# Kernel optimization log

Measured on AMD Instinct MI355X. Metric: run time of the kernel, lower is better.

The kernel has to match this reference:

```python
import jax, jax.numpy as jnp
import numpy as np

N_HEADS = 16
BLOCK_SIZE = 256


def _rope(x):
    # x: [B, H, L, d] ; matches torch RotaryPositionalEmbedding (interleave-split then concat)
    B, H, L, d = x.shape
    inv_freq = 1.0 / (10000.0 ** (jnp.arange(0, d, 2, dtype=jnp.float32) / d))
    t = jnp.arange(L, dtype=jnp.float32)[:, None] * inv_freq[None, :]  # [L, d/2]
    cos, sin = jnp.cos(t), jnp.sin(t)
    x1, x2 = x[..., 0::2], x[..., 1::2]
    return jnp.concatenate([x1 * cos - x2 * sin, x2 * cos + x1 * sin], axis=-1)


def setup_inputs() -> dict:
    key = jax.random.key(0)
    k1, k2, k3 = jax.random.split(key, 3)
    B, L, D = 2, 4096, 1024
    x = jax.random.normal(k1, (B, L, D), dtype=jnp.float32)
    Wqkv = jax.random.normal(k2, (3 * D, D), dtype=jnp.float32) * 0.02
    Wout = jax.random.normal(k3, (D, D), dtype=jnp.float32) * 0.02
    return {"x": x, "Wqkv": Wqkv, "Wout": Wout}


def reference(x, Wqkv, Wout):
    H, BS = N_HEADS, BLOCK_SIZE
    B, L, D = x.shape
    HD = D // H
    scale = HD ** (-0.5)
    nb = L // BS

    qkv = (x @ Wqkv.T).reshape(B, L, 3, H, HD).transpose(2, 0, 3, 1, 4)  # [3,B,H,L,HD]
    q, k, v = qkv[0], qkv[1], qkv[2]
    q, k = _rope(q), _rope(k)

    # block-diagonal causal attention: only within-block scores are ever unmasked,
    # and fp32 exp(finfo.min - max) == 0, so blockwise softmax == masked full softmax
    qb = q.reshape(B, H, nb, BS, HD)
    kb = k.reshape(B, H, nb, BS, HD)
    vb = v.reshape(B, H, nb, BS, HD)

    att = jnp.einsum('bhnqd,bhnkd->bhnqk', qb, kb) * scale
    causal = jnp.tril(jnp.ones((BS, BS), dtype=bool))
    att = jnp.where(causal, att, jnp.finfo(att.dtype).min)
    att = jax.nn.softmax(att, axis=-1)  # dropout p=0.0 -> identity

    out = jnp.einsum('bhnqk,bhnkd->bhnqd', att, vb)
    out = out.reshape(B, H, L, HD).transpose(0, 2, 1, 3).reshape(B, L, D)
    return out @ Wout.T
```

## Files before the change

kernel.cpp:

```cpp
#include <hip/hip_runtime.h>
#include <hip/hip_bf16.h>
#include <cstdint>
#include <cstddef>

typedef __hip_bfloat16 bf16;
typedef __attribute__((ext_vector_type(8))) short bf16x8;
typedef __attribute__((ext_vector_type(4))) float floatx4;

static constexpr int Bb = 2;
static constexpr int Ls = 4096;
static constexpr int Dm = 1024;
static constexpr int Hn = 16;
static constexpr int HD = 64;
static constexpr int BS = 256;
static constexpr int QKVROW = 3 * Dm;
static constexpr int KRP = 72;

static constexpr size_t NX  = (size_t)8192 * 1024;
static constexpr size_t NQ  = (size_t)8192 * 3072;
static constexpr size_t NW1 = (size_t)3072 * 1024;
static constexpr size_t NW2 = (size_t)1024 * 1024;

__device__ __forceinline__ void async_load16(const void* g, void* l) {
  __builtin_amdgcn_global_load_lds(
      (__attribute__((address_space(1))) void*)(void*)(g),
      (__attribute__((address_space(3))) void*)(l), 16, 0, 0);
}

__device__ __forceinline__ short f2bf(float f) {
  union { __hip_bfloat16 b; short s; } u;
  u.b = __float2bfloat16(f);
  return u.s;
}

__device__ __forceinline__ float bf2f(short s) {
  union { unsigned u; float f; } v;
  v.u = ((unsigned)(unsigned short)s) << 16;
  return v.f;
}

__device__ __forceinline__ bf16x8 load8(const float* p) {
  const float4 f0 = *(const float4*)(const void*)p;
  const float4 f1 = *(const float4*)(const void*)(p + 4);
  bf16x8 r;
  r[0] = f2bf(f0.x); r[1] = f2bf(f0.y); r[2] = f2bf(f0.z); r[3] = f2bf(f0.w);
  r[4] = f2bf(f1.x); r[5] = f2bf(f1.y); r[6] = f2bf(f1.z); r[7] = f2bf(f1.w);
  return r;
}

__device__ __forceinline__ void storeC(bf16* C, size_t idx, float v) {
  C[idx] = __float2bfloat16(v);
}
__device__ __forceinline__ void storeC(float* C, size_t idx, float v) {
  C[idx] = v;
}

__global__ void cvt3_kernel(const float* __restrict__ x, const float* __restrict__ w1,
                            const float* __restrict__ w2, bf16* __restrict__ xb,
                            bf16* __restrict__ w1b, bf16* __restrict__ w2b) {
  const size_t i = ((size_t)blockIdx.x * 256 + threadIdx.x) * 8;
  if (i < NX) {
    *(bf16x8*)(void*)((short*)(void*)xb + i) = load8(x + i);
  } else if (i < NX + NW1) {
    const size_t k = i - NX;
    *(bf16x8*)(void*)((short*)(void*)w1b + k) = load8(w1 + k);
  } else {
    const size_t k = i - NX - NW1;
    *(bf16x8*)(void*)((short*)(void*)w2b + k) = load8(w2 + k);
  }
}

template <typename TC>
__global__ __launch_bounds__(256) void gemm_bt_async(
    const bf16* __restrict__ A, const bf16* __restrict__ Bm, TC* __restrict__ C,
    int M, int N, int K) {
  __shared__ __align__(16) short sA[128 * 32];
  __shared__ __align__(16) short sB[128 * 32];
  const int tid  = threadIdx.x;
  const int wave = tid >> 6, lane = tid & 63;
  const int quad = lane >> 4, l15 = lane & 15;
  const int tm = blockIdx.y * 128, tn = blockIdx.x * 128;
  const int wm = (wave >> 1) * 64, wn = (wave & 1) * 64;

  floatx4 acc[4][4];
#pragma unroll
  for (int i = 0; i < 4; i++)
#pragma unroll
    for (int j = 0; j < 4; j++) acc[i][j] = {0.f, 0.f, 0.f, 0.f};

  const int srow = tid >> 2;
  const int scol = (tid & 3) * 8;
  const bf16* Ag0 = A + (size_t)(tm + srow) * K + scol;
  const bf16* Ag1 = A + (size_t)(tm + srow + 64) * K + scol;
  const bf16* Bg0 = Bm + (size_t)(tn + srow) * K + scol;
  const bf16* Bg1 = Bm + (size_t)(tn + srow + 64) * K + scol;
  short* sAd0 = sA + tid * 8;
  short* sAd1 = sA + 2048 + tid * 8;
  short* sBd0 = sB + tid * 8;
  short* sBd1 = sB + 2048 + tid * 8;

  for (int kb = 0; kb < K; kb += 32) {
    __syncthreads();
    async_load16(Ag0 + kb, sAd0);
    async_load16(Ag1 + kb, sAd1);
    async_load16(Bg0 + kb, sBd0);
    async_load16(Bg1 + kb, sBd1);
    __syncthreads();

    bf16x8 af[4], bfr[4];
#pragma unroll
    for (int i = 0; i < 4; i++)
      af[i] = *(const bf16x8*)(sA + (wm + i * 16 + l15) * 32 + quad * 8);
#pragma unroll
    for (int j = 0; j < 4; j++)
      bfr[j] = *(const bf16x8*)(sB + (wn + j * 16 + l15) * 32 + quad * 8);
#pragma unroll
    for (int i = 0; i < 4; i++)
#pragma unroll
      for (int j = 0; j < 4; j++)
        acc[i][j] = __builtin_amdgcn_mfma_f32_16x16x32_bf16(af[i], bfr[j], acc[i][j], 0, 0, 0);
  }

#pragma unroll
  for (int i = 0; i < 4; i++)
#pragma unroll
    for (int j = 0; j < 4; j++)
#pragma unroll
      for (int r = 0; r < 4; r++) {
        const int row = tm + wm + i * 16 + quad * 4 + r;
        const int col = tn + wn + j * 16 + l15;
        storeC(C, (size_t)row * N + col, acc[i][j][r]);
      }
}

__device__ __forceinline__ void rope_frag(const bf16* __restrict__ row, int quad,
                                          float l_pos, const float* __restrict__ freq8,
                                          bf16x8* f0, bf16x8* f1) {
  const bf16x8 w0 = *(const bf16x8*)(const void*)(row + quad * 16);
  const bf16x8 w1 = *(const bf16x8*)(const void*)(row + quad * 16 + 8);
#pragma unroll
  for (int j = 0; j < 8; j++) {
    const short s1 = (j < 4) ? w0[2 * j] : w1[2 * (j - 4)];
    const short s2 = (j < 4) ? w0[2 * j + 1] : w1[2 * (j - 4) + 1];
    const float x1 = bf2f(s1), x2 = bf2f(s2);
    const float rev = l_pos * freq8[j];
    const float fr = rev - floorf(rev);
    const float c = __builtin_amdgcn_cosf(fr);
    const float s = __builtin_amdgcn_sinf(fr);
    (*f0)[j] = f2bf(x1 * c - x2 * s);
    (*f1)[j] = f2bf(x2 * c + x1 * s);
  }
}

__global__ __launch_bounds__(256) void attn_kernel(const bf16* __restrict__ qkv,
                                                   bf16* __restrict__ aout) {
  constexpr float SCALE = 0.125f;
  constexpr float LOG2E = 1.4426950408889634f;
  constexpr float INV2PI = 0.15915494309189535f;
  __shared__ __align__(16) short vT[HD * BS];
  __shared__ __align__(16) short kR[BS * KRP];
  __shared__ __align__(16) short pS[4][16 * 64];
  const int blk = blockIdx.x, h = blockIdx.y, b = blockIdx.z;
  const int tid = threadIdx.x;
  const int wave = tid >> 6, lane = tid & 63;
  const int quad = lane >> 4, l15 = lane & 15;
  const size_t row0 = (size_t)(b * Ls + blk * BS);
  const bf16* qkvR = qkv + row0 * QKVROW;

  float freq8[8];
#pragma unroll
  for (int j = 0; j < 8; j++)
    freq8[j] = exp2f(-13.287712379549449f * (float)(2 * (quad * 8 + j)) * (1.0f / 64.0f))
               * INV2PI;

  {
    const bf16* vrow = qkvR + (size_t)tid * QKVROW + 2 * Dm + h * HD;
#pragma unroll
    for (int i = 0; i < 8; i++) {
      bf16x8 vv = *(const bf16x8*)(vrow + i * 8);
#pragma unroll
      for (int e = 0; e < 8; e++) vT[(i * 8 + e) * BS + tid] = vv[e];
    }
  }

  {
    const bf16* krow = qkvR + (size_t)tid * QKVROW + Dm + h * HD;
    bf16x8 kw[8];
#pragma unroll
    for (int t = 0; t < 8; t++) kw[t] = *(const bf16x8*)(krow + t * 8);
    const float pos = (float)(blk * BS + tid);
    short tmp[64];
#pragma unroll
    for (int i = 0; i < 32; i++) {
      const float x1 = bf2f(kw[(2 * i) >> 3][(2 * i) & 7]);
      const float x2 = bf2f(kw[(2 * i + 1) >> 3][(2 * i + 1) & 7]);
      const float fq = exp2f(-13.287712379549449f * (float)(2 * i) * (1.0f / 64.0f)) * INV2PI;
      const float rev = pos * fq;
      const float fr = rev - floorf(rev);
      const float c = __builtin_amdgcn_cosf(fr);
      const float s = __builtin_amdgcn_sinf(fr);
      tmp[i]      = f2bf(x1 * c - x2 * s);
      tmp[i + 32] = f2bf(x2 * c + x1 * s);
    }
#pragma unroll
    for (int t = 0; t < 8; t++)
      *(bf16x8*)(kR + tid * KRP + t * 8) = *(const bf16x8*)(tmp + t * 8);
  }
  __syncthreads();

  short* myP = &pS[wave][0];

  for (int sp = 0; sp < 2; sp++) {
    const int s = sp ? (7 - wave) : wave;
    const int qrow0 = s * 32;
    const int kcmax = s >> 1;

    bf16x8 qf[2][2];
#pragma unroll
    for (int mt = 0; mt < 2; mt++) {
      const int qr = qrow0 + mt * 16 + l15;
      rope_frag(qkvR + (size_t)qr * QKVROW + h * HD, quad,
                (float)(blk * BS + qr), freq8, &qf[mt][0], &qf[mt][1]);
    }

    float m_i[2][4], l_i[2][4];
    floatx4 o[2][4];
#pragma unroll
    for (int mt = 0; mt < 2; mt++)
#pragma unroll
      for (int r = 0; r < 4; r++) { m_i[mt][r] = -1e30f; l_i[mt][r] = 0.f; }
#pragma unroll
    for (int mt = 0; mt < 2; mt++)
#pragma unroll
      for (int nt = 0; nt < 4; nt++) o[mt][nt] = {0.f, 0.f, 0.f, 0.f};

    for (int kc = 0; kc <= kcmax; kc++) {
      floatx4 sc[2][4];
#pragma unroll
      for (int mt = 0; mt < 2; mt++)
#pragma unroll
        for (int nt = 0; nt < 4; nt++) sc[mt][nt] = {0.f, 0.f, 0.f, 0.f};

      bf16x8 kf[4][2];
#pragma unroll
      for (int nt = 0; nt < 4; nt++) {
        const short* kr = kR + (kc * 64 + nt * 16 + l15) * KRP;
        kf[nt][0] = *(const bf16x8*)(kr + quad * 8);
        kf[nt][1] = *(const bf16x8*)(kr + 32 + quad * 8);
      }

#pragma unroll
      for (int mt = 0; mt < 2; mt++)
#pragma unroll
        for (int nt = 0; nt < 4; nt++) {
          sc[mt][nt] = __builtin_amdgcn_mfma_f32_16x16x32_bf16(qf[mt][0], kf[nt][0], sc[mt][nt], 0, 0, 0);
          sc[mt][nt] = __builtin_amdgcn_mfma_f32_16x16x32_bf16(qf[mt][1], kf[nt][1], sc[mt][nt], 0, 0, 0);
        }

      const bool diag = (kc == kcmax);
#pragma unroll
      for (int mt = 0; mt < 2; mt++)
#pragma unroll
        for (int r = 0; r < 4; r++) {
          const int rowg = qrow0 + mt * 16 + quad * 4 + r;
          float cmax = -1e30f;
#pragma unroll
          for (int nt = 0; nt < 4; nt++) {
            float sv = sc[mt][nt][r] * SCALE;
            if (diag && (kc * 64 + nt * 16 + l15 > rowg)) sv = -1e30f;
            sc[mt][nt][r] = sv;
            cmax = fmaxf(cmax, sv);
          }
#pragma unroll
          for (int off = 1; off < 16; off <<= 1)
            cmax = fmaxf(cmax, __shfl_xor(cmax, off, 64));
          const float mold = m_i[mt][r];
          const float mnew = fmaxf(mold, cmax);
          const float alpha = exp2f((mold - mnew) * LOG2E);
          float rsum = 0.f;
#pragma unroll
          for (int nt = 0; nt < 4; nt++) {
            const float p = exp2f((sc[mt][nt][r] - mnew) * LOG2E);
            sc[mt][nt][r] = p;
            rsum += p;
          }
#pragma unroll
          for (int off = 1; off < 16; off <<= 1)
            rsum += __shfl_xor(rsum, off, 64);
          l_i[mt][r] = l_i[mt][r] * alpha + rsum;
          m_i[mt][r] = mnew;
#pragma unroll
          for (int nt = 0; nt < 4; nt++) o[mt][nt][r] *= alpha;
        }

      bf16x8 vf0[4], vf1[4];
#pragma unroll
      for (int nt = 0; nt < 4; nt++) {
        vf0[nt] = *(const bf16x8*)(vT + (nt * 16 + l15) * BS + kc * 64 + quad * 8);
        vf1[nt] = *(const bf16x8*)(vT + (nt * 16 + l15) * BS + kc * 64 + 32 + quad * 8);
      }

#pragma unroll
      for (int mt = 0; mt < 2; mt++) {
#pragma unroll
        for (int nt = 0; nt < 4; nt++)
#pragma unroll
          for (int r = 0; r < 4; r++)
            myP[(quad * 4 + r) * 64 + nt * 16 + l15] = f2bf(sc[mt][nt][r]);
        __asm__ __volatile__("s_waitcnt lgkmcnt(0)" ::: "memory");
        const bf16x8 pf0 = *(const bf16x8*)(myP + l15 * 64 + quad * 8);
        const bf16x8 pf1 = *(const bf16x8*)(myP + l15 * 64 + 32 + quad * 8);
#pragma unroll
        for (int nt = 0; nt < 4; nt++) {
          o[mt][nt] = __builtin_amdgcn_mfma_f32_16x16x32_bf16(pf0, vf0[nt], o[mt][nt], 0, 0, 0);
          o[mt][nt] = __builtin_amdgcn_mfma_f32_16x16x32_bf16(pf1, vf1[nt], o[mt][nt], 0, 0, 0);
        }
        __asm__ __volatile__("s_waitcnt lgkmcnt(0)" ::: "memory");
      }
    }

#pragma unroll
    for (int mt = 0; mt < 2; mt++)
#pragma unroll
      for (int r = 0; r < 4; r++) {
        const float inv = 1.0f / l_i[mt][r];
#pragma unroll
        for (int nt = 0; nt < 4; nt++) {
          const size_t m = row0 + qrow0 + mt * 16 + quad * 4 + r;
          aout[m * Dm + h * HD + nt * 16 + l15] = __float2bfloat16(o[mt][nt][r] * inv);
        }
      }
  }
}

extern "C" void kernel_launch(void* const* d_in, const int* in_sizes, int n_in,
                              void* d_out, int out_size, void* d_ws, size_t ws_size,
                              hipStream_t stream) {
  const float* x    = (const float*)d_in[0];
  const float* Wqkv = (const float*)d_in[1];
  const float* Wout = (const float*)d_in[2];
  float* out = (float*)d_out;

  bf16* xb    = (bf16*)d_ws;
  bf16* qkv   = xb + NX;
  bf16* Wqkvb = qkv + NQ;
  bf16* Woutb = Wqkvb + NW1;
  bf16* attnb = xb;

  cvt3_kernel<<<(NX + NW1 + NW2) / 2048, 256, 0, stream>>>(x, Wqkv, Wout, xb, Wqkvb, Woutb);

  gemm_bt_async<bf16>
      <<<dim3(3072 / 128, 8192 / 128), 256, 0, stream>>>(xb, Wqkvb, qkv, 8192, 3072, 1024);
  attn_kernel<<<dim3(Ls / BS, Hn, Bb), 256, 0, stream>>>(qkv, attnb);
  gemm_bt_async<float>
      <<<dim3(1024 / 128, 8192 / 128), 256, 0, stream>>>(attnb, Woutb, out, 8192, 1024, 1024);
}
```

Before: 234.0 us.

## Rewrite GEMM with 256x128 tiles, triple-buffered async LDS loads and XOR swizzle

The bf16 GEMM used for the QKV and output projections is replaced. The new version uses 512-thread blocks with 256x128 output tiles and a K-step of 64. It keeps three LDS buffers and prefetches two stages ahead, using vmcnt waits and a single barrier per iteration in place of two full syncs. It also XOR-swizzles the LDS layout to avoid bank conflicts and raises wave priority around the MFMA block. The aim is to hide global-load latency and cut barrier and bank-conflict stalls, at the cost of more LDS per block (about 144KB), which may limit occupancy.

```diff
diff --git a/kernel.cpp b/kernel.cpp
--- a/kernel.cpp
+++ b/kernel.cpp
@@ -71,16 +71,38 @@
 }
 
 template <typename TC>
-__global__ __launch_bounds__(256) void gemm_bt_async(
+__global__ __launch_bounds__(512, 2) void gemm_bt_256(
     const bf16* __restrict__ A, const bf16* __restrict__ Bm, TC* __restrict__ C,
     int M, int N, int K) {
-  __shared__ __align__(16) short sA[128 * 32];
-  __shared__ __align__(16) short sB[128 * 32];
-  const int tid  = threadIdx.x;
+  constexpr int BM = 256, BN = 128, BK = 64, NBUF = 3;
+  __shared__ __align__(16) short sA[NBUF][BM * BK];
+  __shared__ __align__(16) short sB[NBUF][BN * BK];
+  const int tid = threadIdx.x;
   const int wave = tid >> 6, lane = tid & 63;
   const int quad = lane >> 4, l15 = lane & 15;
-  const int tm = blockIdx.y * 128, tn = blockIdx.x * 128;
-  const int wm = (wave >> 1) * 64, wn = (wave & 1) * 64;
+  const int wr = wave >> 1, wc = wave & 1;
+  const int tm = blockIdx.y * BM, tn = blockIdx.x * BN;
+  const int xr = (l15 & 7) << 3;
+
+  const int srow = tid >> 3;
+  const int scol = ((tid & 7) ^ (srow & 7)) * 8;
+  const bf16* Ag = A + (size_t)(tm + srow) * K + scol;
+  const bf16* Bg = Bm + (size_t)(tn + srow) * K + scol;
+  short* sAst = &sA[0][0] + tid * 8;
+  short* sBst = &sB[0][0] + tid * 8;
+
+#define STAGE(T, BUF)                                              \
+  do {                                                             \
+    const size_t kb_ = (size_t)(T) * BK;                           \
+    short* sa_ = sAst + (BUF) * (BM * BK);                         \
+    short* sb_ = sBst + (BUF) * (BN * BK);                         \
+    async_load16(Ag + kb_,                   sa_);                 \
+    async_load16(Ag + kb_ + (size_t)64 * K,  sa_ + 4096);          \
+    async_load16(Ag + kb_ + (size_t)128 * K, sa_ + 8192);          \
+    async_load16(Ag + kb_ + (size_t)192 * K, sa_ + 12288);         \
+    async_load16(Bg + kb_,                   sb_);                 \
+    async_load16(Bg + kb_ + (size_t)64 * K,  sb_ + 4096);          \
+  } while (0)
 
   floatx4 acc[4][4];
 #pragma unroll
@@ -88,48 +110,61 @@
 #pragma unroll
     for (int j = 0; j < 4; j++) acc[i][j] = {0.f, 0.f, 0.f, 0.f};
 
-  const int srow = tid >> 2;
-  const int scol = (tid & 3) * 8;
-  const bf16* Ag0 = A + (size_t)(tm + srow) * K + scol;
-  const bf16* Ag1 = A + (size_t)(tm + srow + 64) * K + scol;
-  const bf16* Bg0 = Bm + (size_t)(tn + srow) * K + scol;
-  const bf16* Bg1 = Bm + (size_t)(tn + srow + 64) * K + scol;
-  short* sAd0 = sA + tid * 8;
-  short* sAd1 = sA + 2048 + tid * 8;
-  short* sBd0 = sB + tid * 8;
-  short* sBd1 = sB + 2048 + tid * 8;
-
-  for (int kb = 0; kb < K; kb += 32) {
-    __syncthreads();
-    async_load16(Ag0 + kb, sAd0);
-    async_load16(Ag1 + kb, sAd1);
-    async_load16(Bg0 + kb, sBd0);
-    async_load16(Bg1 + kb, sBd1);
-    __syncthreads();
-
-    bf16x8 af[4], bfr[4];
-#pragma unroll
-    for (int i = 0; i < 4; i++)
-      af[i] = *(const bf16x8*)(sA + (wm + i * 16 + l15) * 32 + quad * 8);
-#pragma unroll
-    for (int j = 0; j < 4; j++)
-      bfr[j] = *(const bf16x8*)(sB + (wn + j * 16 + l15) * 32 + quad * 8);
-#pragma unroll
-    for (int i = 0; i < 4; i++)
-#pragma unroll
-      for (int j = 0; j < 4; j++)
-        acc[i][j] = __builtin_amdgcn_mfma_f32_16x16x32_bf16(af[i], bfr[j], acc[i][j], 0, 0, 0);
-  }
-
-#pragma unroll
-  for (int i = 0; i < 4; i++)
-#pragma unroll
-    for (int j = 0; j < 4; j++)
+  const int nk = K / BK;
+  STAGE(0, 0);
+  STAGE(1, 1);
+  int cur = 0;
+  for (int t = 0; t < nk; ++t) {
+    if (t + 1 < nk)
+      asm volatile("s_waitcnt vmcnt(6)" ::: "memory");
+    else
+      asm volatile("s_waitcnt vmcnt(0)" ::: "memory");
+    __builtin_amdgcn_s_barrier();
+    if (t + 2 < nk) {
+      int pb = cur + 2; if (pb >= NBUF) pb -= NBUF;
+      STAGE(t + 2, pb);
+    }
+
+    const short* aB = &sA[cur][0];
+    const short* bB = &sB[cur][0];
+    bf16x8 af[4][2], bfr[4][2];
+#pragma unroll
+    for (int m = 0; m < 4; m++) {
+      const int row = wr * 64 + m * 16 + l15;
+#pragma unroll
+      for (int ks = 0; ks < 2; ks++)
+        af[m][ks] = *(const bf16x8*)(aB + ((row * 64 + ks * 32 + quad * 8) ^ xr));
+    }
+#pragma unroll
+    for (int n = 0; n < 4; n++) {
+      const int row = wc * 64 + n * 16 + l15;
+#pragma unroll
+      for (int ks = 0; ks < 2; ks++)
+        bfr[n][ks] = *(const bf16x8*)(bB + ((row * 64 + ks * 32 + quad * 8) ^ xr));
+    }
+
+    __builtin_amdgcn_s_setprio(1);
+#pragma unroll
+    for (int m = 0; m < 4; m++)
+#pragma unroll
+      for (int n = 0; n < 4; n++) {
+        acc[m][n] = __builtin_amdgcn_mfma_f32_16x16x32_bf16(af[m][0], bfr[n][0], acc[m][n], 0, 0, 0);
+        acc[m][n] = __builtin_amdgcn_mfma_f32_16x16x32_bf16(af[m][1], bfr[n][1], acc[m][n], 0, 0, 0);
+      }
+    __builtin_amdgcn_s_setprio(0);
+    cur = (cur == NBUF - 1) ? 0 : cur + 1;
+  }
+#undef STAGE
+
+#pragma unroll
+  for (int m = 0; m < 4; m++)
+#pragma unroll
+    for (int n = 0; n < 4; n++)
 #pragma unroll
       for (int r = 0; r < 4; r++) {
-        const int row = tm + wm + i * 16 + quad * 4 + r;
-        const int col = tn + wn + j * 16 + l15;
-        storeC(C, (size_t)row * N + col, acc[i][j][r]);
+        const int row = tm + wr * 64 + m * 16 + quad * 4 + r;
+        const int col = tn + wc * 64 + n * 16 + l15;
+        storeC(C, (size_t)row * N + col, acc[m][n][r]);
       }
 }
 
@@ -349,9 +384,9 @@
 
   cvt3_kernel<<<(NX + NW1 + NW2) / 2048, 256, 0, stream>>>(x, Wqkv, Wout, xb, Wqkvb, Woutb);
 
-  gemm_bt_async<bf16>
-      <<<dim3(3072 / 128, 8192 / 128), 256, 0, stream>>>(xb, Wqkvb, qkv, 8192, 3072, 1024);
+  gemm_bt_256<bf16>
+      <<<dim3(3072 / 128, 8192 / 256), 512, 0, stream>>>(xb, Wqkvb, qkv, 8192, 3072, 1024);
   attn_kernel<<<dim3(Ls / BS, Hn, Bb), 256, 0, stream>>>(qkv, attnb);
-  gemm_bt_async<float>
-      <<<dim3(1024 / 128, 8192 / 128), 256, 0, stream>>>(attnb, Woutb, out, 8192, 1024, 1024);
-}
+  gemm_bt_256<float>
+      <<<dim3(1024 / 128, 8192 / 256), 512, 0, stream>>>(attnb, Woutb, out, 8192, 1024, 1024);
+}
```

Result: no change. 232.7 us (-0.5%).

## Replace GEMM with 8-wave double-buffered swizzled ping-pong kernel

Applied to the files above, without the earlier changes.

Replaces the 128x128 single-buffered GEMM with a 256x128 tile, 512-thread kernel using BK=64. Shared memory is double-buffered and XOR-swizzled, with async global-to-LDS loads interleaved against MFMA sub-blocks through explicit vmcnt waits, barriers and setprio. The aim is to overlap memory latency with compute, remove LDS bank conflicts and raise arithmetic intensity. In exchange it uses more LDS per block, relies on hand-tuned waitcnt counts for correctness, and launches fewer blocks.

```diff
diff --git a/kernel.cpp b/kernel.cpp
--- a/kernel.cpp
+++ b/kernel.cpp
@@ -71,66 +71,163 @@
 }
 
 template <typename TC>
-__global__ __launch_bounds__(256) void gemm_bt_async(
+__global__ __launch_bounds__(512, 2) void gemm_8p(
     const bf16* __restrict__ A, const bf16* __restrict__ Bm, TC* __restrict__ C,
     int M, int N, int K) {
-  __shared__ __align__(16) short sA[128 * 32];
-  __shared__ __align__(16) short sB[128 * 32];
-  const int tid  = threadIdx.x;
+  constexpr int BK = 64;
+  __shared__ __align__(16) short sA[2][2][128 * 64];
+  __shared__ __align__(16) short sB[2][2][64 * 64];
+  const int tid = threadIdx.x;
   const int wave = tid >> 6, lane = tid & 63;
   const int quad = lane >> 4, l15 = lane & 15;
-  const int tm = blockIdx.y * 128, tn = blockIdx.x * 128;
-  const int wm = (wave >> 1) * 64, wn = (wave & 1) * 64;
+  const int wr = wave >> 1, wc = wave & 1;
+  const int tm = blockIdx.y * 256, tn = blockIdx.x * 128;
+
+  const int iLo = tid >> 3;
+  const int csP = tid & 7;
+  const int csL = csP ^ (iLo & 7);
+  const bf16* gA[2][2];
+  const bf16* gB[2];
+#pragma unroll
+  for (int mi = 0; mi < 2; mi++) {
+#pragma unroll
+    for (int j = 0; j < 2; j++) {
+      const int i = iLo + j * 64;
+      const int r = (i >> 5) * 64 + mi * 32 + (i & 31);
+      gA[mi][j] = A + (size_t)(tm + r) * K + csL * 8;
+    }
+    const int rB = (iLo >> 5) * 64 + mi * 32 + (iLo & 31);
+    gB[mi] = Bm + (size_t)(tn + rB) * K + csL * 8;
+  }
+
+#define STA(nb, mi, kb)                                                     \
+  do {                                                                      \
+    async_load16(gA[mi][0] + (kb), &sA[nb][mi][0] + tid * 8);               \
+    async_load16(gA[mi][1] + (kb), &sA[nb][mi][0] + 4096 + tid * 8);        \
+  } while (0)
+#define STB(nb, ni, kb)                                                     \
+  do {                                                                      \
+    async_load16(gB[ni] + (kb), &sB[nb][ni][0] + tid * 8);                  \
+  } while (0)
+#define BARR()                                                              \
+  do {                                                                      \
+    asm volatile("" ::: "memory");                                          \
+    __builtin_amdgcn_s_barrier();                                           \
+    asm volatile("" ::: "memory");                                          \
+  } while (0)
+#define RDA(buf, mi)                                                        \
+  do {                                                                      \
+    const short* _p = &sA[buf][mi][0];                                      \
+    _Pragma("unroll") for (int m = 0; m < 2; m++)                           \
+        _Pragma("unroll") for (int ks = 0; ks < 2; ks++)                    \
+            af[m][ks] = *(const bf16x8*)(_p + (wr * 32 + m * 16 + l15) * 64 \
+                              + ((ks * 4 + quad) ^ (l15 & 7)) * 8);         \
+  } while (0)
+#define RDB(buf, ni)                                                        \
+  do {                                                                      \
+    const short* _p = &sB[buf][ni][0];                                      \
+    _Pragma("unroll") for (int n = 0; n < 2; n++)                           \
+        _Pragma("unroll") for (int ks = 0; ks < 2; ks++)                    \
+            bfr[n][ks] = *(const bf16x8*)(_p + (wc * 32 + n * 16 + l15) * 64 \
+                              + ((ks * 4 + quad) ^ (l15 & 7)) * 8);         \
+  } while (0)
+#define MM8(mi, ni)                                                         \
+  do {                                                                      \
+    __builtin_amdgcn_s_setprio(1);                                          \
+    _Pragma("unroll") for (int m = 0; m < 2; m++)                           \
+        _Pragma("unroll") for (int n = 0; n < 2; n++) {                     \
+      acc[(mi)*2 + m][(ni)*2 + n] = __builtin_amdgcn_mfma_f32_16x16x32_bf16( \
+          af[m][0], bfr[n][0], acc[(mi)*2 + m][(ni)*2 + n], 0, 0, 0);       \
+      acc[(mi)*2 + m][(ni)*2 + n] = __builtin_amdgcn_mfma_f32_16x16x32_bf16( \
+          af[m][1], bfr[n][1], acc[(mi)*2 + m][(ni)*2 + n], 0, 0, 0);       \
+    }                                                                       \
+    __builtin_amdgcn_s_setprio(0);                                          \
+  } while (0)
 
   floatx4 acc[4][4];
 #pragma unroll
   for (int i = 0; i < 4; i++)
 #pragma unroll
     for (int j = 0; j < 4; j++) acc[i][j] = {0.f, 0.f, 0.f, 0.f};
-
-  const int srow = tid >> 2;
-  const int scol = (tid & 3) * 8;
-  const bf16* Ag0 = A + (size_t)(tm + srow) * K + scol;
-  const bf16* Ag1 = A + (size_t)(tm + srow + 64) * K + scol;
-  const bf16* Bg0 = Bm + (size_t)(tn + srow) * K + scol;
-  const bf16* Bg1 = Bm + (size_t)(tn + srow + 64) * K + scol;
-  short* sAd0 = sA + tid * 8;
-  short* sAd1 = sA + 2048 + tid * 8;
-  short* sBd0 = sB + tid * 8;
-  short* sBd1 = sB + 2048 + tid * 8;
-
-  for (int kb = 0; kb < K; kb += 32) {
-    __syncthreads();
-    async_load16(Ag0 + kb, sAd0);
-    async_load16(Ag1 + kb, sAd1);
-    async_load16(Bg0 + kb, sBd0);
-    async_load16(Bg1 + kb, sBd1);
-    __syncthreads();
-
-    bf16x8 af[4], bfr[4];
-#pragma unroll
-    for (int i = 0; i < 4; i++)
-      af[i] = *(const bf16x8*)(sA + (wm + i * 16 + l15) * 32 + quad * 8);
-#pragma unroll
-    for (int j = 0; j < 4; j++)
-      bfr[j] = *(const bf16x8*)(sB + (wn + j * 16 + l15) * 32 + quad * 8);
-#pragma unroll
-    for (int i = 0; i < 4; i++)
-#pragma unroll
-      for (int j = 0; j < 4; j++)
-        acc[i][j] = __builtin_amdgcn_mfma_f32_16x16x32_bf16(af[i], bfr[j], acc[i][j], 0, 0, 0);
-  }
-
-#pragma unroll
-  for (int i = 0; i < 4; i++)
-#pragma unroll
-    for (int j = 0; j < 4; j++)
-#pragma unroll
-      for (int r = 0; r < 4; r++) {
-        const int row = tm + wm + i * 16 + quad * 4 + r;
-        const int col = tn + wn + j * 16 + l15;
-        storeC(C, (size_t)row * N + col, acc[i][j][r]);
-      }
+  bf16x8 af[2][2], bfr[2][2];
+
+  const int nk = K / BK;
+
+  STB(0, 1, 0);
+  STA(0, 0, 0);
+  STB(0, 0, 0);
+  STA(0, 1, 0);
+
+  for (int t = 0; t < nk - 1; ++t) {
+    const int buf = t & 1, nb = buf ^ 1;
+    const int kb2 = (t + 1) * BK;
+    STB(nb, 1, kb2);
+    asm volatile("s_waitcnt vmcnt(4)" ::: "memory");
+    BARR();
+    RDA(buf, 0);
+    RDB(buf, 1);
+    MM8(0, 1);
+    BARR();
+    STA(nb, 0, kb2);
+    asm volatile("s_waitcnt vmcnt(5)" ::: "memory");
+    BARR();
+    RDB(buf, 0);
+    MM8(0, 0);
+    BARR();
+    STB(nb, 0, kb2);
+    asm volatile("s_waitcnt vmcnt(4)" ::: "memory");
+    BARR();
+    RDA(buf, 1);
+    MM8(1, 0);
+    BARR();
+    STA(nb, 1, kb2);
+    BARR();
+    RDB(buf, 1);
+    MM8(1, 1);
+    BARR();
+  }
+  {
+    const int buf = (nk - 1) & 1;
+    asm volatile("s_waitcnt vmcnt(3)" ::: "memory");
+    BARR();
+    RDA(buf, 0);
+    RDB(buf, 1);
+    MM8(0, 1);
+    BARR();
+    asm volatile("s_waitcnt vmcnt(2)" ::: "memory");
+    BARR();
+    RDB(buf, 0);
+    MM8(0, 0);
+    BARR();
+    asm volatile("s_waitcnt vmcnt(0)" ::: "memory");
+    BARR();
+    RDA(buf, 1);
+    MM8(1, 0);
+    BARR();
+    RDB(buf, 1);
+    MM8(1, 1);
+  }
+#undef STA
+#undef STB
+#undef BARR
+#undef RDA
+#undef RDB
+#undef MM8
+
+#pragma unroll
+  for (int mi = 0; mi < 2; mi++)
+#pragma unroll
+    for (int m = 0; m < 2; m++)
+#pragma unroll
+      for (int ni = 0; ni < 2; ni++)
+#pragma unroll
+        for (int n = 0; n < 2; n++)
+#pragma unroll
+          for (int r = 0; r < 4; r++) {
+            const int row = tm + wr * 64 + mi * 32 + m * 16 + quad * 4 + r;
+            const int col = tn + wc * 64 + ni * 32 + n * 16 + l15;
+            storeC(C, (size_t)row * N + col, acc[mi * 2 + m][ni * 2 + n][r]);
+          }
 }
 
 __device__ __forceinline__ void rope_frag(const bf16* __restrict__ row, int quad,
@@ -349,9 +446,9 @@
 
   cvt3_kernel<<<(NX + NW1 + NW2) / 2048, 256, 0, stream>>>(x, Wqkv, Wout, xb, Wqkvb, Woutb);
 
-  gemm_bt_async<bf16>
-      <<<dim3(3072 / 128, 8192 / 128), 256, 0, stream>>>(xb, Wqkvb, qkv, 8192, 3072, 1024);
+  gemm_8p<bf16>
+      <<<dim3(3072 / 128, 8192 / 256), 512, 0, stream>>>(xb, Wqkvb, qkv, 8192, 3072, 1024);
   attn_kernel<<<dim3(Ls / BS, Hn, Bb), 256, 0, stream>>>(qkv, attnb);
-  gemm_bt_async<float>
-      <<<dim3(1024 / 128, 8192 / 128), 256, 0, stream>>>(attnb, Woutb, out, 8192, 1024, 1024);
-}
+  gemm_8p<float>
+      <<<dim3(1024 / 128, 8192 / 256), 512, 0, stream>>>(attnb, Woutb, out, 8192, 1024, 1024);
+}
```

After: 249.9 us. 1.07x slower.

## Replace GEMM with 8-wave triple-buffered swizzled-LDS pipelined kernel

Applied to the files above, without the earlier changes.

Rewrites the bf16 GEMM used for the QKV and output projections as a 512-thread, 256x128-tile kernel. It uses a BK=64 K-step, triple-buffered LDS with XOR-swizzled layout, and async global-to-LDS prefetch two stages ahead, interleaved with MFMA phases using setprio and explicit waitcnts. The aim is to hide global load latency and cut LDS bank conflicts compared with the previous single-buffered 32-wide K loop that used two syncthreads per step. In exchange it needs much more LDS per block (about 144KB), which limits occupancy, and it relies on hand-tuned barrier and vmcnt sequencing that must be correct for the buffers to rotate safely.

```diff
diff --git a/kernel.cpp b/kernel.cpp
--- a/kernel.cpp
+++ b/kernel.cpp
@@ -71,65 +71,157 @@
 }
 
 template <typename TC>
-__global__ __launch_bounds__(256) void gemm_bt_async(
+__global__ __launch_bounds__(512, 2) void gemm_8p(
     const bf16* __restrict__ A, const bf16* __restrict__ Bm, TC* __restrict__ C,
     int M, int N, int K) {
-  __shared__ __align__(16) short sA[128 * 32];
-  __shared__ __align__(16) short sB[128 * 32];
-  const int tid  = threadIdx.x;
+  constexpr int BK = 64;
+  __shared__ __align__(16) short sA[3][256 * 64];
+  __shared__ __align__(16) short sB[3][128 * 64];
+  const int tid = threadIdx.x;
   const int wave = tid >> 6, lane = tid & 63;
   const int quad = lane >> 4, l15 = lane & 15;
-  const int tm = blockIdx.y * 128, tn = blockIdx.x * 128;
-  const int wm = (wave >> 1) * 64, wn = (wave & 1) * 64;
+  const int wr = wave >> 1, wc = wave & 1;
+  const int tm = blockIdx.y * 256, tn = blockIdx.x * 128;
+
+  const int iLo = tid >> 3;
+  const int csP = tid & 7;
+  const int csL = csP ^ (iLo & 7);
+  const bf16* gA[4];
+  const bf16* gB[2];
+#pragma unroll
+  for (int j = 0; j < 4; j++) gA[j] = A + (size_t)(tm + iLo + 64 * j) * K + csL * 8;
+#pragma unroll
+  for (int j = 0; j < 2; j++) gB[j] = Bm + (size_t)(tn + iLo + 64 * j) * K + csL * 8;
+
+  short* aC  = &sA[0][0];
+  short* aN1 = &sA[1][0];
+  short* aN2 = &sA[2][0];
+  short* bC  = &sB[0][0];
+  short* bN1 = &sB[1][0];
+  short* bN2 = &sB[2][0];
+
+#define STH1(aD, bD, kb)                                   \
+  do {                                                     \
+    async_load16(gA[0] + (kb), (aD) + tid * 8);            \
+    async_load16(gA[1] + (kb), (aD) + 4096 + tid * 8);     \
+    async_load16(gB[0] + (kb), (bD) + tid * 8);            \
+  } while (0)
+#define STH2(aD, bD, kb)                                   \
+  do {                                                     \
+    async_load16(gA[2] + (kb), (aD) + 8192 + tid * 8);     \
+    async_load16(gA[3] + (kb), (aD) + 12288 + tid * 8);    \
+    async_load16(gB[1] + (kb), (bD) + 4096 + tid * 8);     \
+  } while (0)
+#define BARR()                                             \
+  do {                                                     \
+    asm volatile("" ::: "memory");                         \
+    __builtin_amdgcn_s_barrier();                          \
+    asm volatile("" ::: "memory");                         \
+  } while (0)
+#define LGKM0() asm volatile("s_waitcnt lgkmcnt(0)" ::: "memory")
+#define RDB4(bP)                                                               \
+  do {                                                                         \
+    _Pragma("unroll") for (int n = 0; n < 4; n++)                              \
+        _Pragma("unroll") for (int ks = 0; ks < 2; ks++)                       \
+            bfr[n][ks] = *(const bf16x8*)((bP) + (wc * 64 + n * 16 + l15) * 64 \
+                              + ((ks * 4 + quad) ^ (l15 & 7)) * 8);            \
+  } while (0)
+#define RDA2(aP, mh)                                                           \
+  do {                                                                         \
+    _Pragma("unroll") for (int mm = 0; mm < 2; mm++)                           \
+        _Pragma("unroll") for (int ks = 0; ks < 2; ks++)                       \
+            af[mm][ks] = *(const bf16x8*)(                                     \
+                (aP) + (wr * 64 + ((mh)*2 + mm) * 16 + l15) * 64               \
+                + ((ks * 4 + quad) ^ (l15 & 7)) * 8);                          \
+  } while (0)
+#define MM16(mh)                                                               \
+  do {                                                                         \
+    __builtin_amdgcn_s_setprio(1);                                             \
+    _Pragma("unroll") for (int mm = 0; mm < 2; mm++)                           \
+        _Pragma("unroll") for (int n = 0; n < 4; n++) {                        \
+      acc[(mh)*2 + mm][n] = __builtin_amdgcn_mfma_f32_16x16x32_bf16(           \
+          af[mm][0], bfr[n][0], acc[(mh)*2 + mm][n], 0, 0, 0);                 \
+      acc[(mh)*2 + mm][n] = __builtin_amdgcn_mfma_f32_16x16x32_bf16(           \
+          af[mm][1], bfr[n][1], acc[(mh)*2 + mm][n], 0, 0, 0);                 \
+    }                                                                          \
+    __builtin_amdgcn_s_setprio(0);                                             \
+  } while (0)
 
   floatx4 acc[4][4];
 #pragma unroll
   for (int i = 0; i < 4; i++)
 #pragma unroll
     for (int j = 0; j < 4; j++) acc[i][j] = {0.f, 0.f, 0.f, 0.f};
-
-  const int srow = tid >> 2;
-  const int scol = (tid & 3) * 8;
-  const bf16* Ag0 = A + (size_t)(tm + srow) * K + scol;
-  const bf16* Ag1 = A + (size_t)(tm + srow + 64) * K + scol;
-  const bf16* Bg0 = Bm + (size_t)(tn + srow) * K + scol;
-  const bf16* Bg1 = Bm + (size_t)(tn + srow + 64) * K + scol;
-  short* sAd0 = sA + tid * 8;
-  short* sAd1 = sA + 2048 + tid * 8;
-  short* sBd0 = sB + tid * 8;
-  short* sBd1 = sB + 2048 + tid * 8;
-
-  for (int kb = 0; kb < K; kb += 32) {
-    __syncthreads();
-    async_load16(Ag0 + kb, sAd0);
-    async_load16(Ag1 + kb, sAd1);
-    async_load16(Bg0 + kb, sBd0);
-    async_load16(Bg1 + kb, sBd1);
-    __syncthreads();
-
-    bf16x8 af[4], bfr[4];
-#pragma unroll
-    for (int i = 0; i < 4; i++)
-      af[i] = *(const bf16x8*)(sA + (wm + i * 16 + l15) * 32 + quad * 8);
-#pragma unroll
-    for (int j = 0; j < 4; j++)
-      bfr[j] = *(const bf16x8*)(sB + (wn + j * 16 + l15) * 32 + quad * 8);
-#pragma unroll
-    for (int i = 0; i < 4; i++)
-#pragma unroll
-      for (int j = 0; j < 4; j++)
-        acc[i][j] = __builtin_amdgcn_mfma_f32_16x16x32_bf16(af[i], bfr[j], acc[i][j], 0, 0, 0);
-  }
-
-#pragma unroll
-  for (int i = 0; i < 4; i++)
-#pragma unroll
-    for (int j = 0; j < 4; j++)
+  bf16x8 af[2][2], bfr[4][2];
+
+  const int nk = K / BK;
+
+  STH1(aC, bC, 0);
+  STH2(aC, bC, 0);
+  STH1(aN1, bN1, BK);
+  STH2(aN1, bN1, BK);
+  asm volatile("s_waitcnt vmcnt(6)" ::: "memory");
+  BARR();
+
+  for (int t = 0; t < nk - 2; ++t) {
+    const int kb2 = (t + 2) * BK;
+    RDB4(bC);
+    RDA2(aC, 0);
+    STH1(aN2, bN2, kb2);
+    BARR();
+    LGKM0();
+    MM16(0);
+    BARR();
+    RDA2(aC, 1);
+    STH2(aN2, bN2, kb2);
+    asm volatile("s_waitcnt vmcnt(6)" ::: "memory");
+    BARR();
+    LGKM0();
+    MM16(1);
+    BARR();
+    short* ta = aC; aC = aN1; aN1 = aN2; aN2 = ta;
+    short* tb = bC; bC = bN1; bN1 = bN2; bN2 = tb;
+  }
+  RDB4(bC);
+  RDA2(aC, 0);
+  BARR();
+  LGKM0();
+  MM16(0);
+  BARR();
+  RDA2(aC, 1);
+  asm volatile("s_waitcnt vmcnt(0)" ::: "memory");
+  BARR();
+  LGKM0();
+  MM16(1);
+  BARR();
+  {
+    short* ta = aC; aC = aN1; aN1 = aN2; aN2 = ta;
+    short* tb = bC; bC = bN1; bN1 = bN2; bN2 = tb;
+  }
+  RDB4(bC);
+  RDA2(aC, 0);
+  LGKM0();
+  MM16(0);
+  RDA2(aC, 1);
+  LGKM0();
+  MM16(1);
+#undef STH1
+#undef STH2
+#undef BARR
+#undef LGKM0
+#undef RDB4
+#undef RDA2
+#undef MM16
+
+#pragma unroll
+  for (int m = 0; m < 4; m++)
+#pragma unroll
+    for (int n = 0; n < 4; n++)
 #pragma unroll
       for (int r = 0; r < 4; r++) {
-        const int row = tm + wm + i * 16 + quad * 4 + r;
-        const int col = tn + wn + j * 16 + l15;
-        storeC(C, (size_t)row * N + col, acc[i][j][r]);
+        const int row = tm + wr * 64 + m * 16 + quad * 4 + r;
+        const int col = tn + wc * 64 + n * 16 + l15;
+        storeC(C, (size_t)row * N + col, acc[m][n][r]);
       }
 }
 
@@ -349,9 +441,9 @@
 
   cvt3_kernel<<<(NX + NW1 + NW2) / 2048, 256, 0, stream>>>(x, Wqkv, Wout, xb, Wqkvb, Woutb);
 
-  gemm_bt_async<bf16>
-      <<<dim3(3072 / 128, 8192 / 128), 256, 0, stream>>>(xb, Wqkvb, qkv, 8192, 3072, 1024);
+  gemm_8p<bf16>
+      <<<dim3(3072 / 128, 8192 / 256), 512, 0, stream>>>(xb, Wqkvb, qkv, 8192, 3072, 1024);
   attn_kernel<<<dim3(Ls / BS, Hn, Bb), 256, 0, stream>>>(qkv, attnb);
-  gemm_bt_async<float>
-      <<<dim3(1024 / 128, 8192 / 128), 256, 0, stream>>>(attnb, Woutb, out, 8192, 1024, 1024);
-}
+  gemm_8p<float>
+      <<<dim3(1024 / 128, 8192 / 256), 512, 0, stream>>>(attnb, Woutb, out, 8192, 1024, 1024);
+}
```

Result: faster. 214.2 us (-8.4%).
